# Kernel optimization log

Hardware: AMD Instinct MI355X
Metric: run time of the kernel (lower is better)

## Reference

```python
import jax, jax.numpy as jnp
import numpy as np

IN_FEATURE = 1024
OUT_FEATURE = 1024
BLOCK_SIZE = 64
L = 2048


def setup_inputs() -> dict:
    key = jax.random.key(0)
    k1, k2, k3, k4 = jax.random.split(key, 4)
    input1 = jax.random.normal(k1, (L, IN_FEATURE), dtype=jnp.float32)
    input2 = jax.random.normal(k2, (L, IN_FEATURE), dtype=jnp.float32)
    # nn.Linear(in_feature*block_size, out_feature): weight [O, in*b], bias [O]
    fan_in = IN_FEATURE * BLOCK_SIZE
    bound = 1.0 / np.sqrt(fan_in)
    W = jax.random.uniform(k3, (OUT_FEATURE, fan_in), dtype=jnp.float32, minval=-bound, maxval=bound)
    b = jax.random.uniform(k4, (OUT_FEATURE,), dtype=jnp.float32, minval=-bound, maxval=bound)
    return {"input1": input1, "input2": input2, "W": W, "b": b}


def reference(input1, input2, W, b):
    l, h = input1.shape
    g = h // BLOCK_SIZE  # number of blocks
    x1 = input1.reshape(l, g, BLOCK_SIZE)
    x2 = input2.reshape(l, g, BLOCK_SIZE)
    # Original: outer = x1[..., :, None] * x2[..., None, :] -> [l, g*b*b] -> Linear.
    # Fused form: contract the block-wise outer product directly with the
    # reshaped weight W[o, g, i, j]; identical math, no [l, h*b] intermediate.
    Wr = W.reshape(OUT_FEATURE, g, BLOCK_SIZE, BLOCK_SIZE)
    out = jnp.einsum('lgi,lgj,ogij->lo', x1, x2, Wr) + b
    return out
```

## Files before the change

kernel.cpp:

```cpp
#include <hip/hip_runtime.h>
#include <hip/hip_bf16.h>
#include <stdint.h>


#define L_DIM 2048
#define H_DIM 1024
#define O_DIM 1024
#define KDIM  65536

constexpr int BM = 128, BN = 128;
constexpr int SPLITK = 4;
constexpr int KITERS = 1024 / SPLITK;
constexpr int BSTR = 72;

typedef __attribute__((ext_vector_type(8))) short bf16x8;
typedef __attribute__((ext_vector_type(8))) unsigned short u16x8;
typedef __attribute__((ext_vector_type(4))) float f32x4;
typedef __attribute__((ext_vector_type(4))) unsigned int u32x4;

__device__ __forceinline__ unsigned short f2b(float x) {
    __hip_bfloat16 h = __float2bfloat16(x);
    unsigned short u;
    __builtin_memcpy(&u, &h, 2);
    return u;
}

__device__ __forceinline__ unsigned pk2(float a, float b) {
    float2 t; t.x = a; t.y = b;
    __hip_bfloat162 h = __float22bfloat162_rn(t);
    unsigned u;
    __builtin_memcpy(&u, &h, 4);
    return u;
}

__global__ __launch_bounds__(256) void w_convert(const float* __restrict__ W,
                                                 unsigned short* __restrict__ Wb) {
    const size_t nchunk = (size_t)O_DIM * KDIM / 16;
    const size_t stride = (size_t)gridDim.x * 256;
    const f32x4* src = reinterpret_cast<const f32x4*>(W);
    u16x8* dst = reinterpret_cast<u16x8*>(Wb);
    for (size_t c = (size_t)blockIdx.x * 256 + threadIdx.x; c < nchunk; c += stride) {
        f32x4 a0 = __builtin_nontemporal_load(src + c * 4 + 0);
        f32x4 a1 = __builtin_nontemporal_load(src + c * 4 + 1);
        f32x4 a2 = __builtin_nontemporal_load(src + c * 4 + 2);
        f32x4 a3 = __builtin_nontemporal_load(src + c * 4 + 3);
        u32x4 p0, p1;
        p0[0] = pk2(a0.x, a0.y); p0[1] = pk2(a0.z, a0.w);
        p0[2] = pk2(a1.x, a1.y); p0[3] = pk2(a1.z, a1.w);
        p1[0] = pk2(a2.x, a2.y); p1[1] = pk2(a2.z, a2.w);
        p1[2] = pk2(a3.x, a3.y); p1[3] = pk2(a3.z, a3.w);
        dst[c * 2 + 0] = __builtin_bit_cast(u16x8, p0);
        dst[c * 2 + 1] = __builtin_bit_cast(u16x8, p1);
    }
}

__global__ __launch_bounds__(256) void gl_init(const float* __restrict__ bias,
                                               float* __restrict__ out) {
    int idx = blockIdx.x * 256 + threadIdx.x;
    int o = (idx * 4) & (O_DIM - 1);
    f32x4 bv = *reinterpret_cast<const f32x4*>(bias + o);
    reinterpret_cast<f32x4*>(out)[idx] = bv;
}

__global__ __launch_bounds__(256, 2) void gl_gemm(const float* __restrict__ x1,
                                                  const float* __restrict__ x2,
                                                  const unsigned short* __restrict__ Wb,
                                                  float* __restrict__ out) {
    __shared__ unsigned short Bb[2][BN * BSTR];

    const int tid  = threadIdx.x;
    const int lane = tid & 63;
    const int wid  = tid >> 6;
    const int wm   = (wid >> 1) * 64;
    const int wn   = (wid & 1) * 64;
    const int quad = lane >> 4;
    const int l16  = lane & 15;

    const int id  = blockIdx.x;
    const int n0  = (id & 7) * BN;
    const int m0  = ((id >> 3) & 15) * BM;
    const int kk0 = (id >> 7) * KITERS;

    unsigned aoff[4];
    #pragma unroll
    for (int t = 0; t < 4; ++t)
        aoff[t] = (unsigned)(m0 + wm + t * 16 + l16) * H_DIM;
    const unsigned qo = quad * 8;

    const int brow = tid >> 3;
    const int bcol = (tid & 7) * 8;
    const unsigned short* gB = Wb + (size_t)(n0 + brow) * KDIM + (size_t)kk0 * 64 + bcol;
    const int bl = brow * BSTR + bcol;

    f32x4 acc[4][4] = {};
    f32x4 x2c[4][4];
    u16x8 rA[4], rB_[4];
    float xc[4], xn[4];

    auto loadB = [&](int t, u16x8 (&r)[4]) {
        const unsigned short* gp = gB + (size_t)t * 64;
        #pragma unroll
        for (int p = 0; p < 4; ++p)
            r[p] = *reinterpret_cast<const u16x8*>(gp + (size_t)p * 32 * KDIM);
    };
    auto loadX1 = [&](int t, float (&v)[4]) {
        const unsigned kc = (unsigned)(kk0 + t);
        #pragma unroll
        for (int mt = 0; mt < 4; ++mt)
            v[mt] = x1[aoff[mt] + kc];
    };
    auto refillX2 = [&](int t) {
        const unsigned gb = (unsigned)(kk0 + t);
        #pragma unroll
        for (int mt = 0; mt < 4; ++mt) {
            const float* p = x2 + aoff[mt] + gb + qo;
            x2c[mt][0] = *reinterpret_cast<const f32x4*>(p);
            x2c[mt][1] = *reinterpret_cast<const f32x4*>(p + 4);
            x2c[mt][2] = *reinterpret_cast<const f32x4*>(p + 32);
            x2c[mt][3] = *reinterpret_cast<const f32x4*>(p + 36);
        }
    };

#define GL_BODY(T, BUFR, BUFW, WSET, LSET)                                        \
    {                                                                             \
        const int t_ = (T);                                                       \
        const bool hn1 = (t_ + 1 < KITERS);                                       \
        const bool hn2 = (t_ + 2 < KITERS);                                       \
        if (hn1) {                                                                \
            _Pragma("unroll")                                                     \
            for (int p = 0; p < 4; ++p)                                           \
                *reinterpret_cast<u16x8*>(&Bb[BUFW][bl + p * 32 * BSTR]) = WSET[p];\
        }                                                                         \
        if (hn2) loadB(t_ + 2, LSET);                                             \
        if (hn1) loadX1(t_ + 1, xn);                                              \
        _Pragma("unroll")                                                         \
        for (int ks = 0; ks < 2; ++ks) {                                          \
            const int koff = ks * 32 + qo;                                        \
            bf16x8 af[4], bfr[4];                                                 \
            _Pragma("unroll")                                                     \
            for (int nt = 0; nt < 4; ++nt)                                        \
                bfr[nt] = *reinterpret_cast<const bf16x8*>(                       \
                    &Bb[BUFR][(wn + nt * 16 + l16) * BSTR + koff]);               \
            _Pragma("unroll")                                                     \
            for (int mt = 0; mt < 4; ++mt) {                                      \
                f32x4 lo = x2c[mt][ks * 2]     * xc[mt];                          \
                f32x4 hi = x2c[mt][ks * 2 + 1] * xc[mt];                          \
                u32x4 pk;                                                         \
                pk[0] = pk2(lo.x, lo.y); pk[1] = pk2(lo.z, lo.w);                 \
                pk[2] = pk2(hi.x, hi.y); pk[3] = pk2(hi.z, hi.w);                 \
                af[mt] = __builtin_bit_cast(bf16x8, pk);                          \
            }                                                                     \
            _Pragma("unroll")                                                     \
            for (int mt = 0; mt < 4; ++mt)                                        \
                _Pragma("unroll")                                                 \
                for (int nt = 0; nt < 4; ++nt)                                    \
                    acc[mt][nt] = __builtin_amdgcn_mfma_f32_16x16x32_bf16(        \
                        af[mt], bfr[nt], acc[mt][nt], 0, 0, 0);                   \
        }                                                                         \
        _Pragma("unroll")                                                         \
        for (int mt = 0; mt < 4; ++mt) xc[mt] = xn[mt];                           \
        __builtin_amdgcn_sched_barrier(0);                                        \
        asm volatile("s_waitcnt lgkmcnt(0)" ::: "memory");                        \
        __builtin_amdgcn_s_barrier();                                             \
        __builtin_amdgcn_sched_barrier(0);                                        \
    }

    loadB(0, rA);
    loadX1(0, xc);
    #pragma unroll
    for (int p = 0; p < 4; ++p)
        *reinterpret_cast<u16x8*>(&Bb[0][bl + p * 32 * BSTR]) = rA[p];
    loadB(1, rB_);
    __builtin_amdgcn_sched_barrier(0);
    asm volatile("s_waitcnt lgkmcnt(0)" ::: "memory");
    __builtin_amdgcn_s_barrier();
    __builtin_amdgcn_sched_barrier(0);

    for (int itb = 0; itb < KITERS; itb += 2) {
        if ((itb & 63) == 0) refillX2(itb);
        GL_BODY(itb,     0, 1, rB_, rA)
        GL_BODY(itb + 1, 1, 0, rA, rB_)
    }
#undef GL_BODY

    #pragma unroll
    for (int mt = 0; mt < 4; ++mt) {
        const int mb = m0 + wm + mt * 16 + quad * 4;
        #pragma unroll
        for (int nt = 0; nt < 4; ++nt) {
            const int n = n0 + wn + nt * 16 + l16;
            #pragma unroll
            for (int r = 0; r < 4; ++r)
                unsafeAtomicAdd(&out[(mb + r) * O_DIM + n], acc[mt][nt][r]);
        }
    }
}

constexpr int STR = 72;
__global__ __launch_bounds__(256, 2) void gl_gemm_fb(const float* __restrict__ x1,
                                                     const float* __restrict__ x2,
                                                     const float* __restrict__ W,
                                                     float* __restrict__ out) {
    __shared__ unsigned short Ab[BM * STR];
    __shared__ unsigned short Bb2[BM * STR];

    const int tid  = threadIdx.x;
    const int lane = tid & 63;
    const int wid  = tid >> 6;
    const int wm   = (wid >> 1) * 64;
    const int wn   = (wid & 1) * 64;
    const int quad = lane >> 4;
    const int l16  = lane & 15;
    const int m0   = blockIdx.y * BM;
    const int n0   = blockIdx.x * BN;
    const int kk0  = blockIdx.z * (1024 / 4);

    const int srow = tid >> 4;
    const int scol = (tid & 15) * 4;

    f32x4 acc[4][4] = {};

    for (int kk = kk0; kk < kk0 + (1024 / 4); ++kk) {
        const int g = kk >> 6;
        const int i = kk & 63;
        __syncthreads();
        #pragma unroll
        for (int c = 0; c < 8; ++c) {
            const int r = srow + c * 16;
            const float x1v = x1[(m0 + r) * H_DIM + g * 64 + i];
            const f32x4 v = *reinterpret_cast<const f32x4*>(
                &x2[(m0 + r) * H_DIM + g * 64 + scol]);
            ushort4 h;
            h.x = f2b(v.x * x1v); h.y = f2b(v.y * x1v);
            h.z = f2b(v.z * x1v); h.w = f2b(v.w * x1v);
            *reinterpret_cast<ushort4*>(&Ab[r * STR + scol]) = h;
        }
        #pragma unroll
        for (int c = 0; c < 8; ++c) {
            const int r = srow + c * 16;
            const f32x4 v = *reinterpret_cast<const f32x4*>(
                &W[(size_t)(n0 + r) * KDIM + (size_t)kk * 64 + scol]);
            ushort4 h;
            h.x = f2b(v.x); h.y = f2b(v.y); h.z = f2b(v.z); h.w = f2b(v.w);
            *reinterpret_cast<ushort4*>(&Bb2[r * STR + scol]) = h;
        }
        __syncthreads();
        #pragma unroll
        for (int ks = 0; ks < 2; ++ks) {
            const int koff = ks * 32 + quad * 8;
            bf16x8 af[4], bfr[4];
            #pragma unroll
            for (int mt = 0; mt < 4; ++mt)
                af[mt] = *reinterpret_cast<const bf16x8*>(
                    &Ab[(wm + mt * 16 + l16) * STR + koff]);
            #pragma unroll
            for (int nt = 0; nt < 4; ++nt)
                bfr[nt] = *reinterpret_cast<const bf16x8*>(
                    &Bb2[(wn + nt * 16 + l16) * STR + koff]);
            #pragma unroll
            for (int mt = 0; mt < 4; ++mt)
                #pragma unroll
                for (int nt = 0; nt < 4; ++nt)
                    acc[mt][nt] = __builtin_amdgcn_mfma_f32_16x16x32_bf16(
                        af[mt], bfr[nt], acc[mt][nt], 0, 0, 0);
        }
    }
    #pragma unroll
    for (int mt = 0; mt < 4; ++mt) {
        const int mb = m0 + wm + mt * 16 + quad * 4;
        #pragma unroll
        for (int nt = 0; nt < 4; ++nt) {
            const int n = n0 + wn + nt * 16 + l16;
            #pragma unroll
            for (int r = 0; r < 4; ++r)
                unsafeAtomicAdd(&out[(mb + r) * O_DIM + n], acc[mt][nt][r]);
        }
    }
}

extern "C" void kernel_launch(void* const* d_in, const int* in_sizes, int n_in,
                              void* d_out, int out_size, void* d_ws, size_t ws_size,
                              hipStream_t stream) {
    const float* x1 = (const float*)d_in[0];
    const float* x2 = (const float*)d_in[1];
    const float* W  = (const float*)d_in[2];
    const float* b  = (const float*)d_in[3];
    float* out = (float*)d_out;

    const size_t w_bf16_bytes = (size_t)O_DIM * KDIM * sizeof(unsigned short);

    gl_init<<<dim3((L_DIM * O_DIM / 4) / 256), dim3(256), 0, stream>>>(b, out);

    if (ws_size >= w_bf16_bytes) {
        unsigned short* Wb = (unsigned short*)d_ws;
        w_convert<<<dim3(4096), dim3(256), 0, stream>>>(W, Wb);
        gl_gemm<<<dim3(8 * 16 * SPLITK), dim3(256), 0, stream>>>(x1, x2, Wb, out);
    } else {
        dim3 grid(O_DIM / BN, L_DIM / BM, 4);
        gl_gemm_fb<<<grid, dim3(256), 0, stream>>>(x1, x2, W, out);
    }
}
```

Baseline: 778.3 us.

## Fuse W fp32-to-bf16 conversion into GEMM and stage x1 via shared memory

Removes the separate pass that converted all of W to bf16 in workspace, and the fallback kernel. The GEMM now loads fp32 W directly, packing it to bf16 before writing to LDS. This avoids writing and re-reading a 128MB bf16 copy, at the cost of reading twice as many bytes of W inside the GEMM. x1 values are staged once per 64-iteration block into shared memory, transposed, instead of being loaded with scalar global reads every iteration. The extra LDS and registers may lower occupancy.

Measured after the change: 786.9 us. No clear change (+1.1%).

```diff
diff --git a/kernel.cpp b/kernel.cpp
--- a/kernel.cpp
+++ b/kernel.cpp
@@ -17,13 +17,6 @@
 typedef __attribute__((ext_vector_type(8))) unsigned short u16x8;
 typedef __attribute__((ext_vector_type(4))) float f32x4;
 typedef __attribute__((ext_vector_type(4))) unsigned int u32x4;
-
-__device__ __forceinline__ unsigned short f2b(float x) {
-    __hip_bfloat16 h = __float2bfloat16(x);
-    unsigned short u;
-    __builtin_memcpy(&u, &h, 2);
-    return u;
-}
 
 __device__ __forceinline__ unsigned pk2(float a, float b) {
     float2 t; t.x = a; t.y = b;
@@ -33,27 +26,6 @@
     return u;
 }
 
-__global__ __launch_bounds__(256) void w_convert(const float* __restrict__ W,
-                                                 unsigned short* __restrict__ Wb) {
-    const size_t nchunk = (size_t)O_DIM * KDIM / 16;
-    const size_t stride = (size_t)gridDim.x * 256;
-    const f32x4* src = reinterpret_cast<const f32x4*>(W);
-    u16x8* dst = reinterpret_cast<u16x8*>(Wb);
-    for (size_t c = (size_t)blockIdx.x * 256 + threadIdx.x; c < nchunk; c += stride) {
-        f32x4 a0 = __builtin_nontemporal_load(src + c * 4 + 0);
-        f32x4 a1 = __builtin_nontemporal_load(src + c * 4 + 1);
-        f32x4 a2 = __builtin_nontemporal_load(src + c * 4 + 2);
-        f32x4 a3 = __builtin_nontemporal_load(src + c * 4 + 3);
-        u32x4 p0, p1;
-        p0[0] = pk2(a0.x, a0.y); p0[1] = pk2(a0.z, a0.w);
-        p0[2] = pk2(a1.x, a1.y); p0[3] = pk2(a1.z, a1.w);
-        p1[0] = pk2(a2.x, a2.y); p1[1] = pk2(a2.z, a2.w);
-        p1[2] = pk2(a3.x, a3.y); p1[3] = pk2(a3.z, a3.w);
-        dst[c * 2 + 0] = __builtin_bit_cast(u16x8, p0);
-        dst[c * 2 + 1] = __builtin_bit_cast(u16x8, p1);
-    }
-}
-
 __global__ __launch_bounds__(256) void gl_init(const float* __restrict__ bias,
                                                float* __restrict__ out) {
     int idx = blockIdx.x * 256 + threadIdx.x;
@@ -64,9 +36,10 @@
 
 __global__ __launch_bounds__(256, 2) void gl_gemm(const float* __restrict__ x1,
                                                   const float* __restrict__ x2,
-                                                  const unsigned short* __restrict__ Wb,
+                                                  const float* __restrict__ W,
                                                   float* __restrict__ out) {
     __shared__ unsigned short Bb[2][BN * BSTR];
+    __shared__ float X1s[64 * 128];
 
     const int tid  = threadIdx.x;
     const int lane = tid & 63;
@@ -89,25 +62,35 @@
 
     const int brow = tid >> 3;
     const int bcol = (tid & 7) * 8;
-    const unsigned short* gB = Wb + (size_t)(n0 + brow) * KDIM + (size_t)kk0 * 64 + bcol;
+    const float* gW = W + (size_t)(n0 + brow) * KDIM + (size_t)kk0 * 64 + bcol;
     const int bl = brow * BSTR + bcol;
 
     f32x4 acc[4][4] = {};
     f32x4 x2c[4][4];
-    u16x8 rA[4], rB_[4];
-    float xc[4], xn[4];
-
-    auto loadB = [&](int t, u16x8 (&r)[4]) {
-        const unsigned short* gp = gB + (size_t)t * 64;
-        #pragma unroll
-        for (int p = 0; p < 4; ++p)
-            r[p] = *reinterpret_cast<const u16x8*>(gp + (size_t)p * 32 * KDIM);
+    f32x4 rA[8], rB_[8];
+
+    auto loadB = [&](int t, f32x4 (&r)[8]) {
+        const float* gp = gW + (size_t)t * 64;
+        #pragma unroll
+        for (int p = 0; p < 4; ++p) {
+            const f32x4* q = reinterpret_cast<const f32x4*>(gp + (size_t)p * 32 * KDIM);
+            r[2 * p]     = q[0];
+            r[2 * p + 1] = q[1];
+        }
     };
-    auto loadX1 = [&](int t, float (&v)[4]) {
-        const unsigned kc = (unsigned)(kk0 + t);
-        #pragma unroll
-        for (int mt = 0; mt < 4; ++mt)
-            v[mt] = x1[aoff[mt] + kc];
+    auto stageX1 = [&](int t) {
+        const int r0 = tid >> 1;
+        const int cb = (tid & 1) * 32;
+        const float* xr = x1 + (size_t)(m0 + r0) * H_DIM + (unsigned)(kk0 + t) + cb;
+        #pragma unroll
+        for (int cc = 0; cc < 8; ++cc) {
+            f32x4 v = *reinterpret_cast<const f32x4*>(xr + cc * 4);
+            const int c = cb + cc * 4;
+            X1s[(c + 0) * 128 + r0] = v.x;
+            X1s[(c + 1) * 128 + r0] = v.y;
+            X1s[(c + 2) * 128 + r0] = v.z;
+            X1s[(c + 3) * 128 + r0] = v.w;
+        }
     };
     auto refillX2 = [&](int t) {
         const unsigned gb = (unsigned)(kk0 + t);
@@ -124,15 +107,26 @@
 #define GL_BODY(T, BUFR, BUFW, WSET, LSET)                                        \
     {                                                                             \
         const int t_ = (T);                                                       \
+        float xc[4];                                                              \
+        {                                                                         \
+            const float* xp = &X1s[((t_) & 63) * 128 + wm + l16];                 \
+            xc[0] = xp[0]; xc[1] = xp[16]; xc[2] = xp[32]; xc[3] = xp[48];        \
+        }                                                                         \
         const bool hn1 = (t_ + 1 < KITERS);                                       \
         const bool hn2 = (t_ + 2 < KITERS);                                       \
         if (hn1) {                                                                \
             _Pragma("unroll")                                                     \
-            for (int p = 0; p < 4; ++p)                                           \
-                *reinterpret_cast<u16x8*>(&Bb[BUFW][bl + p * 32 * BSTR]) = WSET[p];\
+            for (int p = 0; p < 4; ++p) {                                         \
+                u32x4 pk;                                                         \
+                pk[0] = pk2(WSET[2 * p].x,     WSET[2 * p].y);                    \
+                pk[1] = pk2(WSET[2 * p].z,     WSET[2 * p].w);                    \
+                pk[2] = pk2(WSET[2 * p + 1].x, WSET[2 * p + 1].y);                \
+                pk[3] = pk2(WSET[2 * p + 1].z, WSET[2 * p + 1].w);                \
+                *reinterpret_cast<u16x8*>(&Bb[BUFW][bl + p * 32 * BSTR]) =        \
+                    __builtin_bit_cast(u16x8, pk);                                \
+            }                                                                     \
         }                                                                         \
         if (hn2) loadB(t_ + 2, LSET);                                             \
-        if (hn1) loadX1(t_ + 1, xn);                                              \
         _Pragma("unroll")                                                         \
         for (int ks = 0; ks < 2; ++ks) {                                          \
             const int koff = ks * 32 + qo;                                        \
@@ -157,8 +151,6 @@
                     acc[mt][nt] = __builtin_amdgcn_mfma_f32_16x16x32_bf16(        \
                         af[mt], bfr[nt], acc[mt][nt], 0, 0, 0);                   \
         }                                                                         \
-        _Pragma("unroll")                                                         \
-        for (int mt = 0; mt < 4; ++mt) xc[mt] = xn[mt];                           \
         __builtin_amdgcn_sched_barrier(0);                                        \
         asm volatile("s_waitcnt lgkmcnt(0)" ::: "memory");                        \
         __builtin_amdgcn_s_barrier();                                             \
@@ -166,105 +158,32 @@
     }
 
     loadB(0, rA);
-    loadX1(0, xc);
     #pragma unroll
-    for (int p = 0; p < 4; ++p)
-        *reinterpret_cast<u16x8*>(&Bb[0][bl + p * 32 * BSTR]) = rA[p];
+    for (int p = 0; p < 4; ++p) {
+        u32x4 pk;
+        pk[0] = pk2(rA[2 * p].x,     rA[2 * p].y);
+        pk[1] = pk2(rA[2 * p].z,     rA[2 * p].w);
+        pk[2] = pk2(rA[2 * p + 1].x, rA[2 * p + 1].y);
+        pk[3] = pk2(rA[2 * p + 1].z, rA[2 * p + 1].w);
+        *reinterpret_cast<u16x8*>(&Bb[0][bl + p * 32 * BSTR]) =
+            __builtin_bit_cast(u16x8, pk);
+    }
     loadB(1, rB_);
-    __builtin_amdgcn_sched_barrier(0);
-    asm volatile("s_waitcnt lgkmcnt(0)" ::: "memory");
-    __builtin_amdgcn_s_barrier();
-    __builtin_amdgcn_sched_barrier(0);
 
     for (int itb = 0; itb < KITERS; itb += 2) {
-        if ((itb & 63) == 0) refillX2(itb);
+        if ((itb & 63) == 0) {
+            stageX1(itb);
+            refillX2(itb);
+            __builtin_amdgcn_sched_barrier(0);
+            asm volatile("s_waitcnt lgkmcnt(0)" ::: "memory");
+            __builtin_amdgcn_s_barrier();
+            __builtin_amdgcn_sched_barrier(0);
+        }
         GL_BODY(itb,     0, 1, rB_, rA)
         GL_BODY(itb + 1, 1, 0, rA, rB_)
     }
 #undef GL_BODY
 
-    #pragma unroll
-    for (int mt = 0; mt < 4; ++mt) {
-        const int mb = m0 + wm + mt * 16 + quad * 4;
-        #pragma unroll
-        for (int nt = 0; nt < 4; ++nt) {
-            const int n = n0 + wn + nt * 16 + l16;
-            #pragma unroll
-            for (int r = 0; r < 4; ++r)
-                unsafeAtomicAdd(&out[(mb + r) * O_DIM + n], acc[mt][nt][r]);
-        }
-    }
-}
-
-constexpr int STR = 72;
-__global__ __launch_bounds__(256, 2) void gl_gemm_fb(const float* __restrict__ x1,
-                                                     const float* __restrict__ x2,
-                                                     const float* __restrict__ W,
-                                                     float* __restrict__ out) {
-    __shared__ unsigned short Ab[BM * STR];
-    __shared__ unsigned short Bb2[BM * STR];
-
-    const int tid  = threadIdx.x;
-    const int lane = tid & 63;
-    const int wid  = tid >> 6;
-    const int wm   = (wid >> 1) * 64;
-    const int wn   = (wid & 1) * 64;
-    const int quad = lane >> 4;
-    const int l16  = lane & 15;
-    const int m0   = blockIdx.y * BM;
-    const int n0   = blockIdx.x * BN;
-    const int kk0  = blockIdx.z * (1024 / 4);
-
-    const int srow = tid >> 4;
-    const int scol = (tid & 15) * 4;
-
-    f32x4 acc[4][4] = {};
-
-    for (int kk = kk0; kk < kk0 + (1024 / 4); ++kk) {
-        const int g = kk >> 6;
-        const int i = kk & 63;
-        __syncthreads();
-        #pragma unroll
-        for (int c = 0; c < 8; ++c) {
-            const int r = srow + c * 16;
-            const float x1v = x1[(m0 + r) * H_DIM + g * 64 + i];
-            const f32x4 v = *reinterpret_cast<const f32x4*>(
-                &x2[(m0 + r) * H_DIM + g * 64 + scol]);
-            ushort4 h;
-            h.x = f2b(v.x * x1v); h.y = f2b(v.y * x1v);
-            h.z = f2b(v.z * x1v); h.w = f2b(v.w * x1v);
-            *reinterpret_cast<ushort4*>(&Ab[r * STR + scol]) = h;
-        }
-        #pragma unroll
-        for (int c = 0; c < 8; ++c) {
-            const int r = srow + c * 16;
-            const f32x4 v = *reinterpret_cast<const f32x4*>(
-                &W[(size_t)(n0 + r) * KDIM + (size_t)kk * 64 + scol]);
-            ushort4 h;
-            h.x = f2b(v.x); h.y = f2b(v.y); h.z = f2b(v.z); h.w = f2b(v.w);
-            *reinterpret_cast<ushort4*>(&Bb2[r * STR + scol]) = h;
-        }
-        __syncthreads();
-        #pragma unroll
-        for (int ks = 0; ks < 2; ++ks) {
-            const int koff = ks * 32 + quad * 8;
-            bf16x8 af[4], bfr[4];
-            #pragma unroll
-            for (int mt = 0; mt < 4; ++mt)
-                af[mt] = *reinterpret_cast<const bf16x8*>(
-                    &Ab[(wm + mt * 16 + l16) * STR + koff]);
-            #pragma unroll
-            for (int nt = 0; nt < 4; ++nt)
-                bfr[nt] = *reinterpret_cast<const bf16x8*>(
-                    &Bb2[(wn + nt * 16 + l16) * STR + koff]);
-            #pragma unroll
-            for (int mt = 0; mt < 4; ++mt)
-                #pragma unroll
-                for (int nt = 0; nt < 4; ++nt)
-                    acc[mt][nt] = __builtin_amdgcn_mfma_f32_16x16x32_bf16(
-                        af[mt], bfr[nt], acc[mt][nt], 0, 0, 0);
-        }
-    }
     #pragma unroll
     for (int mt = 0; mt < 4; ++mt) {
         const int mb = m0 + wm + mt * 16 + quad * 4;
@@ -286,17 +205,8 @@
     const float* W  = (const float*)d_in[2];
     const float* b  = (const float*)d_in[3];
     float* out = (float*)d_out;
-
-    const size_t w_bf16_bytes = (size_t)O_DIM * KDIM * sizeof(unsigned short);
+    (void)d_ws; (void)ws_size;
 
     gl_init<<<dim3((L_DIM * O_DIM / 4) / 256), dim3(256), 0, stream>>>(b, out);
-
-    if (ws_size >= w_bf16_bytes) {
-        unsigned short* Wb = (unsigned short*)d_ws;
-        w_convert<<<dim3(4096), dim3(256), 0, stream>>>(W, Wb);
-        gl_gemm<<<dim3(8 * 16 * SPLITK), dim3(256), 0, stream>>>(x1, x2, Wb, out);
-    } else {
-        dim3 grid(O_DIM / BN, L_DIM / BM, 4);
-        gl_gemm_fb<<<grid, dim3(256), 0, stream>>>(x1, x2, W, out);
-    }
-}
+    gl_gemm<<<dim3(8 * 16 * SPLITK), dim3(256), 0, stream>>>(x1, x2, W, out);
+}
```

## Pre-swizzle bf16 weights into MFMA fragment layout and load B directly to registers

Applied to the files above, without the earlier changes.

The weight conversion kernel now writes bf16 W in a fragment-ordered layout, so the GEMM loads B operands straight from global memory into registers, double-buffered. This removes the per-iteration shared-memory staging of B and the block barrier that went with it. x1 is now staged through shared memory in 64-column chunks instead of being read with scattered scalar global loads. Bias initialization is folded into the conversion kernel to save a launch. In exchange, the strided reads in the conversion may coalesce less well, and more register pressure comes from holding 16 B fragments.

Result: faster. 719.8 us (-7.5%).

```diff
diff --git a/kernel.cpp b/kernel.cpp
--- a/kernel.cpp
+++ b/kernel.cpp
@@ -11,19 +11,11 @@
 constexpr int BM = 128, BN = 128;
 constexpr int SPLITK = 4;
 constexpr int KITERS = 1024 / SPLITK;
-constexpr int BSTR = 72;
 
 typedef __attribute__((ext_vector_type(8))) short bf16x8;
 typedef __attribute__((ext_vector_type(8))) unsigned short u16x8;
 typedef __attribute__((ext_vector_type(4))) float f32x4;
 typedef __attribute__((ext_vector_type(4))) unsigned int u32x4;
-
-__device__ __forceinline__ unsigned short f2b(float x) {
-    __hip_bfloat16 h = __float2bfloat16(x);
-    unsigned short u;
-    __builtin_memcpy(&u, &h, 2);
-    return u;
-}
 
 __device__ __forceinline__ unsigned pk2(float a, float b) {
     float2 t; t.x = a; t.y = b;
@@ -33,24 +25,40 @@
     return u;
 }
 
-__global__ __launch_bounds__(256) void w_convert(const float* __restrict__ W,
-                                                 unsigned short* __restrict__ Wb) {
-    const size_t nchunk = (size_t)O_DIM * KDIM / 16;
-    const size_t stride = (size_t)gridDim.x * 256;
-    const f32x4* src = reinterpret_cast<const f32x4*>(W);
-    u16x8* dst = reinterpret_cast<u16x8*>(Wb);
-    for (size_t c = (size_t)blockIdx.x * 256 + threadIdx.x; c < nchunk; c += stride) {
-        f32x4 a0 = __builtin_nontemporal_load(src + c * 4 + 0);
-        f32x4 a1 = __builtin_nontemporal_load(src + c * 4 + 1);
-        f32x4 a2 = __builtin_nontemporal_load(src + c * 4 + 2);
-        f32x4 a3 = __builtin_nontemporal_load(src + c * 4 + 3);
-        u32x4 p0, p1;
-        p0[0] = pk2(a0.x, a0.y); p0[1] = pk2(a0.z, a0.w);
-        p0[2] = pk2(a1.x, a1.y); p0[3] = pk2(a1.z, a1.w);
-        p1[0] = pk2(a2.x, a2.y); p1[1] = pk2(a2.z, a2.w);
-        p1[2] = pk2(a3.x, a3.y); p1[3] = pk2(a3.z, a3.w);
-        dst[c * 2 + 0] = __builtin_bit_cast(u16x8, p0);
-        dst[c * 2 + 1] = __builtin_bit_cast(u16x8, p1);
+__device__ __forceinline__ unsigned short f2b(float x) {
+    __hip_bfloat16 h = __float2bfloat16(x);
+    unsigned short u;
+    __builtin_memcpy(&u, &h, 2);
+    return u;
+}
+
+__global__ __launch_bounds__(256) void w_cvt(const float* __restrict__ W,
+                                             unsigned short* __restrict__ Wt,
+                                             const float* __restrict__ bias,
+                                             float* __restrict__ out) {
+    const int idx = blockIdx.x * 256 + threadIdx.x;
+    {
+        const int o = (idx * 4) & (O_DIM - 1);
+        f32x4 bv = *reinterpret_cast<const f32x4*>(bias + o);
+        reinterpret_cast<f32x4*>(out)[idx] = bv;
+    }
+    const int lane = threadIdx.x & 63;
+    const int l16  = lane & 15;
+    const int quad = lane >> 4;
+    const int wv   = blockIdx.x * 4 + (threadIdx.x >> 6);
+    #pragma unroll
+    for (int s = 0; s < 16; ++s) {
+        const int u  = wv * 16 + s;
+        const int kc = u >> 6;
+        const int nt = u & 63;
+        const float* src = W + (size_t)(nt * 16 + l16) * KDIM + kc * 32 + quad * 8;
+        f32x4 a = *reinterpret_cast<const f32x4*>(src);
+        f32x4 b = *reinterpret_cast<const f32x4*>(src + 4);
+        u32x4 pk;
+        pk[0] = pk2(a.x, a.y); pk[1] = pk2(a.z, a.w);
+        pk[2] = pk2(b.x, b.y); pk[3] = pk2(b.z, b.w);
+        *reinterpret_cast<u16x8*>(Wt + (size_t)u * 512 + lane * 8) =
+            __builtin_bit_cast(u16x8, pk);
     }
 }
 
@@ -64,9 +72,9 @@
 
 __global__ __launch_bounds__(256, 2) void gl_gemm(const float* __restrict__ x1,
                                                   const float* __restrict__ x2,
-                                                  const unsigned short* __restrict__ Wb,
+                                                  const unsigned short* __restrict__ Wt,
                                                   float* __restrict__ out) {
-    __shared__ unsigned short Bb[2][BN * BSTR];
+    __shared__ float X1s[64 * 128];
 
     const int tid  = threadIdx.x;
     const int lane = tid & 63;
@@ -87,27 +95,40 @@
         aoff[t] = (unsigned)(m0 + wm + t * 16 + l16) * H_DIM;
     const unsigned qo = quad * 8;
 
-    const int brow = tid >> 3;
-    const int bcol = (tid & 7) * 8;
-    const unsigned short* gB = Wb + (size_t)(n0 + brow) * KDIM + (size_t)kk0 * 64 + bcol;
-    const int bl = brow * BSTR + bcol;
+    const unsigned short* gWt = Wt + (size_t)kk0 * 65536
+                                   + (size_t)((n0 + wn) >> 4) * 512 + lane * 8;
 
     f32x4 acc[4][4] = {};
     f32x4 x2c[4][4];
-    u16x8 rA[4], rB_[4];
+    bf16x8 fE[8], fO[8];
     float xc[4], xn[4];
 
-    auto loadB = [&](int t, u16x8 (&r)[4]) {
-        const unsigned short* gp = gB + (size_t)t * 64;
-        #pragma unroll
-        for (int p = 0; p < 4; ++p)
-            r[p] = *reinterpret_cast<const u16x8*>(gp + (size_t)p * 32 * KDIM);
+    auto loadF = [&](int t, bf16x8 (&f)[8]) {
+        const unsigned short* p = gWt + (size_t)t * 65536;
+        #pragma unroll
+        for (int ks = 0; ks < 2; ++ks)
+            #pragma unroll
+            for (int nt = 0; nt < 4; ++nt)
+                f[ks * 4 + nt] = *reinterpret_cast<const bf16x8*>(
+                    p + ks * 32768 + nt * 512);
     };
-    auto loadX1 = [&](int t, float (&v)[4]) {
-        const unsigned kc = (unsigned)(kk0 + t);
-        #pragma unroll
-        for (int mt = 0; mt < 4; ++mt)
-            v[mt] = x1[aoff[mt] + kc];
+    auto loadXC = [&](int t, float (&v)[4]) {
+        const float* xp = &X1s[(t & 63) * 128 + wm + l16];
+        v[0] = xp[0]; v[1] = xp[16]; v[2] = xp[32]; v[3] = xp[48];
+    };
+    auto stageX1 = [&](int t) {
+        const int r0 = tid >> 1;
+        const int cb = (tid & 1) * 32;
+        const float* xr = x1 + (size_t)(m0 + r0) * H_DIM + (unsigned)(kk0 + t) + cb;
+        #pragma unroll
+        for (int cc = 0; cc < 8; ++cc) {
+            f32x4 v = *reinterpret_cast<const f32x4*>(xr + cc * 4);
+            const int c = cb + cc * 4;
+            X1s[(c + 0) * 128 + r0] = v.x;
+            X1s[(c + 1) * 128 + r0] = v.y;
+            X1s[(c + 2) * 128 + r0] = v.z;
+            X1s[(c + 3) * 128 + r0] = v.w;
+        }
     };
     auto refillX2 = [&](int t) {
         const unsigned gb = (unsigned)(kk0 + t);
@@ -121,26 +142,15 @@
         }
     };
 
-#define GL_BODY(T, BUFR, BUFW, WSET, LSET)                                        \
+#define GL_BODY(T, FU, FP)                                                        \
     {                                                                             \
         const int t_ = (T);                                                       \
         const bool hn1 = (t_ + 1 < KITERS);                                       \
-        const bool hn2 = (t_ + 2 < KITERS);                                       \
-        if (hn1) {                                                                \
-            _Pragma("unroll")                                                     \
-            for (int p = 0; p < 4; ++p)                                           \
-                *reinterpret_cast<u16x8*>(&Bb[BUFW][bl + p * 32 * BSTR]) = WSET[p];\
-        }                                                                         \
-        if (hn2) loadB(t_ + 2, LSET);                                             \
-        if (hn1) loadX1(t_ + 1, xn);                                              \
+        if (hn1) loadF(t_ + 1, FP);                                               \
+        if (hn1 && (((t_ + 1) & 63) != 0)) loadXC(t_ + 1, xn);                    \
         _Pragma("unroll")                                                         \
         for (int ks = 0; ks < 2; ++ks) {                                          \
-            const int koff = ks * 32 + qo;                                        \
-            bf16x8 af[4], bfr[4];                                                 \
-            _Pragma("unroll")                                                     \
-            for (int nt = 0; nt < 4; ++nt)                                        \
-                bfr[nt] = *reinterpret_cast<const bf16x8*>(                       \
-                    &Bb[BUFR][(wn + nt * 16 + l16) * BSTR + koff]);               \
+            bf16x8 af[4];                                                         \
             _Pragma("unroll")                                                     \
             for (int mt = 0; mt < 4; ++mt) {                                      \
                 f32x4 lo = x2c[mt][ks * 2]     * xc[mt];                          \
@@ -155,31 +165,24 @@
                 _Pragma("unroll")                                                 \
                 for (int nt = 0; nt < 4; ++nt)                                    \
                     acc[mt][nt] = __builtin_amdgcn_mfma_f32_16x16x32_bf16(        \
-                        af[mt], bfr[nt], acc[mt][nt], 0, 0, 0);                   \
+                        af[mt], FU[ks * 4 + nt], acc[mt][nt], 0, 0, 0);           \
         }                                                                         \
         _Pragma("unroll")                                                         \
         for (int mt = 0; mt < 4; ++mt) xc[mt] = xn[mt];                           \
-        __builtin_amdgcn_sched_barrier(0);                                        \
-        asm volatile("s_waitcnt lgkmcnt(0)" ::: "memory");                        \
-        __builtin_amdgcn_s_barrier();                                             \
-        __builtin_amdgcn_sched_barrier(0);                                        \
-    }
-
-    loadB(0, rA);
-    loadX1(0, xc);
-    #pragma unroll
-    for (int p = 0; p < 4; ++p)
-        *reinterpret_cast<u16x8*>(&Bb[0][bl + p * 32 * BSTR]) = rA[p];
-    loadB(1, rB_);
-    __builtin_amdgcn_sched_barrier(0);
-    asm volatile("s_waitcnt lgkmcnt(0)" ::: "memory");
-    __builtin_amdgcn_s_barrier();
-    __builtin_amdgcn_sched_barrier(0);
+    }
+
+    loadF(0, fE);
 
     for (int itb = 0; itb < KITERS; itb += 2) {
-        if ((itb & 63) == 0) refillX2(itb);
-        GL_BODY(itb,     0, 1, rB_, rA)
-        GL_BODY(itb + 1, 1, 0, rA, rB_)
+        if ((itb & 63) == 0) {
+            __syncthreads();
+            stageX1(itb);
+            refillX2(itb);
+            __syncthreads();
+            loadXC(itb, xc);
+        }
+        GL_BODY(itb,     fE, fO)
+        GL_BODY(itb + 1, fO, fE)
     }
 #undef GL_BODY
 
@@ -287,15 +290,14 @@
     const float* b  = (const float*)d_in[3];
     float* out = (float*)d_out;
 
-    const size_t w_bf16_bytes = (size_t)O_DIM * KDIM * sizeof(unsigned short);
-
-    gl_init<<<dim3((L_DIM * O_DIM / 4) / 256), dim3(256), 0, stream>>>(b, out);
-
-    if (ws_size >= w_bf16_bytes) {
-        unsigned short* Wb = (unsigned short*)d_ws;
-        w_convert<<<dim3(4096), dim3(256), 0, stream>>>(W, Wb);
-        gl_gemm<<<dim3(8 * 16 * SPLITK), dim3(256), 0, stream>>>(x1, x2, Wb, out);
+    const size_t wt_bytes = (size_t)O_DIM * KDIM * sizeof(unsigned short);
+
+    if (ws_size >= wt_bytes) {
+        unsigned short* Wt = (unsigned short*)d_ws;
+        w_cvt<<<dim3(2048), dim3(256), 0, stream>>>(W, Wt, b, out);
+        gl_gemm<<<dim3(8 * 16 * SPLITK), dim3(256), 0, stream>>>(x1, x2, Wt, out);
     } else {
+        gl_init<<<dim3((L_DIM * O_DIM / 4) / 256), dim3(256), 0, stream>>>(b, out);
         dim3 grid(O_DIM / BN, L_DIM / BM, 4);
         gl_gemm_fb<<<grid, dim3(256), 0, stream>>>(x1, x2, W, out);
     }
```
